# Kernel tuning notes

Hardware: AMD Instinct MI355X
Metric: run time of the kernel (lower is better)

Reference implementation:

```python
import jax, jax.numpy as jnp
import numpy as np

B, D, R = 16384, 4096, 64       # batch tokens, embed_dim, low_rank_dimension
N_PART = 8                       # number of subspace partitions
P = R // N_PART                  # partition size = 8
N_SEL = 4                        # partitions selected per example


def setup_inputs() -> dict:
    key = jax.random.key(0)
    k1, k2, k3, k4 = jax.random.split(key, 4)
    base = jax.random.normal(k1, (B, D), dtype=jnp.float32)
    source = jax.random.normal(k2, (B, D), dtype=jnp.float32)
    # orthogonal low-rank rotation (torch.nn.utils.parametrizations.orthogonal)
    W, _ = jnp.linalg.qr(jax.random.normal(k3, (D, R), dtype=jnp.float32))  # [D, R], orthonormal cols
    subspaces = jax.random.randint(k4, (B, N_SEL), 0, N_PART)               # partition ids per example
    return {"base": base, "source": source, "W": W, "subspaces": subspaces}


def reference(base, source, W, subspaces):
    # rotate into low-rank space: [B, R]
    rotated_base = base @ W
    rotated_source = source @ W
    diff = rotated_source - rotated_base

    # per-example selected rotated-space indices (contiguous partitions of size P)
    # idx[b] = concat over selected partitions of [p*P, p*P+P)
    idx = (subspaces[:, :, None] * P + jnp.arange(P)).reshape(B, N_SEL * P)  # [B, N_SEL*P]

    # Selecting columns of diff and matching rows of W.T, then matmul, is
    # equivalent to masking unselected rotated dims to zero and doing one GEMM.
    mask = jnp.zeros((B, R), dtype=diff.dtype).at[jnp.arange(B)[:, None], idx].set(1.0)
    output = base + (diff * mask) @ W.T  # [B, D]
    return output.astype(base.dtype)
```

## Files before the change

### kernel.cpp

```cpp
#include <hip/hip_runtime.h>


#define D_DIM 4096
#define R_DIM 64
#define BM1   16
#define BM2   32

typedef short bf16vec8 __attribute__((ext_vector_type(8)));
typedef float f32x4v  __attribute__((ext_vector_type(4)));

__device__ __forceinline__ unsigned int f2bf_u(float f) {
  unsigned int u = __builtin_bit_cast(unsigned int, f);
  return (u + 0x7fffu + ((u >> 16) & 1u)) >> 16;
}
__device__ __forceinline__ unsigned int pack2bf(float a, float b) {
  return f2bf_u(a) | (f2bf_u(b) << 16);
}
__device__ __forceinline__ void async_ld16(const void* g, void* l) {
  __builtin_amdgcn_global_load_lds(
      (const __attribute__((address_space(1))) void*)g,
      (__attribute__((address_space(3))) void*)l, 16, 0, 0);
}

__global__ __launch_bounds__(256)
void lrri_prep(const float* __restrict__ W, unsigned short* __restrict__ Wt,
               unsigned short* __restrict__ Wb) {
  const int idx = blockIdx.x * blockDim.x + threadIdx.x;
  const int k = idx >> 4;
  const int j = (idx & 15) * 4;
  float4 w = *(const float4*)(W + (size_t)k * R_DIM + j);
  ushort4 p;
  p.x = (unsigned short)f2bf_u(w.x);
  p.y = (unsigned short)f2bf_u(w.y);
  p.z = (unsigned short)f2bf_u(w.z);
  p.w = (unsigned short)f2bf_u(w.w);
  *(ushort4*)(Wb + (size_t)k * R_DIM + j) = p;
  Wt[(size_t)(j + 0) * D_DIM + k] = p.x;
  Wt[(size_t)(j + 1) * D_DIM + k] = p.y;
  Wt[(size_t)(j + 2) * D_DIM + k] = p.z;
  Wt[(size_t)(j + 3) * D_DIM + k] = p.w;
}

__global__ __launch_bounds__(512, 8)
void k1_rotdiff(const float* __restrict__ base, const float* __restrict__ srcp,
                const int* __restrict__ subs,
                const unsigned short* __restrict__ Wt_bf,
                unsigned short* __restrict__ rm_g)
{
  __shared__ __align__(16) float part[8][64 * 17];
  const int tid  = threadIdx.x;
  const int wave = tid >> 6;
  const int lane = tid & 63;
  const int l4   = lane & 15;
  const int g    = lane >> 4;
  const long rowbase = (long)blockIdx.x * BM1;
  const long rowA    = (rowbase + l4) * (long)D_DIM;
  const int  kq0     = wave * 512;
  const int  off1    = (blockIdx.x * 5) & 7;

  f32x4v acc[4];
  #pragma unroll
  for (int t = 0; t < 4; ++t) acc[t] = (f32x4v){0.f, 0.f, 0.f, 0.f};

  auto loadd = [&](int c, float4 (&vb)[4], float4 (&vs)[4]) {
    const int ch = (c + off1) & 7;
    const long colf = kq0 + ch * 64;
    #pragma unroll
    for (int q = 0; q < 4; ++q) {
      const long off = rowA + colf + (q >> 1) * 32 + g * 8 + (q & 1) * 4;
      vb[q] = *(const float4*)(base + off);
      vs[q] = *(const float4*)(srcp + off);
    }
  };

  auto comp = [&](int c, const float4 (&vb)[4], const float4 (&vs)[4]) {
    const int ch = (c + off1) & 7;
    const long colf = kq0 + ch * 64;
    uint4 df[2];
    #pragma unroll
    for (int s = 0; s < 2; ++s) {
      float d0 = vs[s*2].x - vb[s*2].x, d1 = vs[s*2].y - vb[s*2].y;
      float d2 = vs[s*2].z - vb[s*2].z, d3 = vs[s*2].w - vb[s*2].w;
      float d4 = vs[s*2+1].x - vb[s*2+1].x, d5 = vs[s*2+1].y - vb[s*2+1].y;
      float d6 = vs[s*2+1].z - vb[s*2+1].z, d7 = vs[s*2+1].w - vb[s*2+1].w;
      df[s].x = pack2bf(d0, d1);
      df[s].y = pack2bf(d2, d3);
      df[s].z = pack2bf(d4, d5);
      df[s].w = pack2bf(d6, d7);
    }
    #pragma unroll
    for (int t = 0; t < 4; ++t) {
      #pragma unroll
      for (int s = 0; s < 2; ++s) {
        uint4 wf = *(const uint4*)(Wt_bf + (size_t)(t * 16 + l4) * D_DIM +
                                   colf + s * 32 + g * 8);
        acc[t] = __builtin_amdgcn_mfma_f32_16x16x32_bf16(
            __builtin_bit_cast(bf16vec8, wf),
            __builtin_bit_cast(bf16vec8, df[s]),
            acc[t], 0, 0, 0);
      }
    }
  };

  float4 b0[4], s0[4], b1[4], s1[4];
  loadd(0, b0, s0);
  loadd(1, b1, s1); comp(0, b0, s0);
  loadd(2, b0, s0); comp(1, b1, s1);
  loadd(3, b1, s1); comp(2, b0, s0);
  loadd(4, b0, s0); comp(3, b1, s1);
  loadd(5, b1, s1); comp(4, b0, s0);
  loadd(6, b0, s0); comp(5, b1, s1);
  loadd(7, b1, s1); comp(6, b0, s0);
  comp(7, b1, s1);

  #pragma unroll
  for (int t = 0; t < 4; ++t)
    #pragma unroll
    for (int i = 0; i < 4; ++i)
      part[wave][(t * 16 + g * 4 + i) * 17 + l4] = acc[t][i];
  __syncthreads();

  {
    const int row = tid >> 5, jg = tid & 31;
    const int j0 = jg * 2;
    int4 sb = *(const int4*)(subs + (rowbase + row) * 4);
    unsigned mbits = (1u << sb.x) | (1u << sb.y) | (1u << sb.z) | (1u << sb.w);
    unsigned short v[2];
    #pragma unroll
    for (int jj = 0; jj < 2; ++jj) {
      const int j = j0 + jj;
      float sum = 0.f;
      #pragma unroll
      for (int w = 0; w < 8; ++w) sum += part[w][j * 17 + row];
      v[jj] = ((mbits >> (j >> 3)) & 1u) ? (unsigned short)f2bf_u(sum)
                                         : (unsigned short)0;
    }
    *(unsigned int*)(rm_g + (rowbase + row) * 64 + j0) =
        (unsigned)v[0] | ((unsigned)v[1] << 16);
  }
}

__global__ __launch_bounds__(256, 4)
void k2_apply(const float* __restrict__ base,
              const unsigned short* __restrict__ rm_g,
              const unsigned short* __restrict__ Wb_bf,
              float* __restrict__ out)
{
  __shared__ __align__(16) unsigned char smem[36864];
  const int tid  = threadIdx.x;
  const int wave = tid >> 6;
  const int lane = tid & 63;
  const int l4   = lane & 15;
  const int g    = lane >> 4;
  const long rowbase = (long)blockIdx.x * BM2;
  const int off2 = (blockIdx.x * 5) & 15;

  uint4 a2[2][2];
  #pragma unroll
  for (int m = 0; m < 2; ++m)
    #pragma unroll
    for (int s = 0; s < 2; ++s)
      a2[m][s] = *(const uint4*)(rm_g + (rowbase + m * 16 + l4) * 64 +
                                 s * 32 + g * 8);

  float* cbuf = (float*)(smem + wave * 9216);
  #pragma unroll 1
  for (int grp = 0; grp < 16; ++grp) {
    const int ga = (grp + off2) & 15;
    const int cbase = wave * 1024 + ga * 64;
    float4 bb[8];
    #pragma unroll
    for (int v2 = 0; v2 < 8; ++v2) {
      const int r = g + v2 * 4;
      bb[v2] = *(const float4*)(base + (rowbase + r) * D_DIM + cbase + l4 * 4);
    }
    f32x4v a[2][4];
    #pragma unroll
    for (int m = 0; m < 2; ++m)
      #pragma unroll
      for (int t = 0; t < 4; ++t) a[m][t] = (f32x4v){0.f, 0.f, 0.f, 0.f};
    #pragma unroll
    for (int t = 0; t < 4; ++t) {
      #pragma unroll
      for (int s = 0; s < 2; ++s) {
        uint4 bfrag = *(const uint4*)(Wb_bf +
            (size_t)(cbase + t * 16 + l4) * R_DIM + s * 32 + g * 8);
        #pragma unroll
        for (int m = 0; m < 2; ++m)
          a[m][t] = __builtin_amdgcn_mfma_f32_16x16x32_bf16(
              __builtin_bit_cast(bf16vec8, a2[m][s]),
              __builtin_bit_cast(bf16vec8, bfrag), a[m][t], 0, 0, 0);
      }
    }
    #pragma unroll
    for (int m = 0; m < 2; ++m)
      #pragma unroll
      for (int t = 0; t < 4; ++t)
        #pragma unroll
        for (int i = 0; i < 4; ++i)
          cbuf[(m * 16 + g * 4 + i) * 72 + t * 16 + l4] = a[m][t][i];
    __syncthreads();
    #pragma unroll
    for (int v2 = 0; v2 < 8; ++v2) {
      const int r = g + v2 * 4;
      f32x4v cv = *(const f32x4v*)(cbuf + r * 72 + l4 * 4);
      float4 o;
      o.x = cv[0] + bb[v2].x;
      o.y = cv[1] + bb[v2].y;
      o.z = cv[2] + bb[v2].z;
      o.w = cv[3] + bb[v2].w;
      *(float4*)(out + (rowbase + r) * D_DIM + cbase + l4 * 4) = o;
    }
    __syncthreads();
  }
}

__global__ __launch_bounds__(256, 2)
void lrri_fused_nows(const float* __restrict__ base, const float* __restrict__ srcp,
                     const float* __restrict__ W, const int* __restrict__ subs,
                     float* __restrict__ out)
{
  __shared__ __align__(16) unsigned char smem[70144];
  const int tid  = threadIdx.x;
  const int wave = tid >> 6;
  const int lane = tid & 63;
  const int l4   = lane & 15;
  const int g    = lane >> 4;
  const int rh   = wave >> 1;
  const int kh   = wave & 1;
  const long rowbase = (long)blockIdx.x * BM2;
  const long rowg    = rowbase + rh * 16;
  unsigned char* wbuf = smem + wave * 16384;
  const int off1 = (blockIdx.x * 7) & 63;
  const int off2 = (blockIdx.x * 5) & 15;

  f32x4v acc[4];
  #pragma unroll
  for (int t = 0; t < 4; ++t) acc[t] = (f32x4v){0.f, 0.f, 0.f, 0.f};

  #pragma unroll 1
  for (int c = 0; c < 64; ++c) {
    const int ch = (c + off1) & 63;
    unsigned char* buf = wbuf + (c & 1) * 8192;
    const long colf = kh * 2048 + ch * 32;
    #pragma unroll
    for (int q = 0; q < 2; ++q) {
      const int r = q * 8 + (lane >> 3);
      const unsigned b = ((unsigned)((lane & 7) * 16)) ^ ((unsigned)(r & 7) << 4);
      const long goff = (rowg + r) * (long)D_DIM + colf + (b >> 2);
      async_ld16(base + goff, buf + q * 1024);
      async_ld16(srcp + goff, buf + 2048 + q * 1024);
    }
    asm volatile("s_waitcnt vmcnt(0)" ::: "memory");
    __builtin_amdgcn_sched_barrier(0);
    const unsigned sw = (unsigned)((l4 & 7) << 4);
    const unsigned c0 = ((unsigned)(g * 32)) ^ sw;
    const unsigned c1 = ((unsigned)(g * 32 + 16)) ^ sw;
    float4 fb0 = *(const float4*)(buf + l4 * 128 + c0);
    float4 fb1 = *(const float4*)(buf + l4 * 128 + c1);
    float4 fs0 = *(const float4*)(buf + 2048 + l4 * 128 + c0);
    float4 fs1 = *(const float4*)(buf + 2048 + l4 * 128 + c1);
    uint4 af;
    af.x = pack2bf(fs0.x - fb0.x, fs0.y - fb0.y);
    af.y = pack2bf(fs0.z - fb0.z, fs0.w - fb0.w);
    af.z = pack2bf(fs1.x - fb1.x, fs1.y - fb1.y);
    af.w = pack2bf(fs1.z - fb1.z, fs1.w - fb1.w);
    #pragma unroll
    for (int t = 0; t < 4; ++t) {
      unsigned int pq[4];
      #pragma unroll
      for (int e2 = 0; e2 < 4; ++e2) {
        float wa = W[(size_t)(colf + g * 8 + e2 * 2    ) * R_DIM + t * 16 + l4];
        float wb = W[(size_t)(colf + g * 8 + e2 * 2 + 1) * R_DIM + t * 16 + l4];
        pq[e2] = pack2bf(wa, wb);
      }
      uint4 wf; wf.x = pq[0]; wf.y = pq[1]; wf.z = pq[2]; wf.w = pq[3];
      acc[t] = __builtin_amdgcn_mfma_f32_16x16x32_bf16(
          __builtin_bit_cast(bf16vec8, af),
          __builtin_bit_cast(bf16vec8, wf), acc[t], 0, 0, 0);
    }
  }

  {
    float* part = (float*)wbuf;
    #pragma unroll
    for (int t = 0; t < 4; ++t)
      #pragma unroll
      for (int i = 0; i < 4; ++i)
        part[(g * 4 + i) * 72 + t * 16 + l4] = acc[t][i];
  }
  __syncthreads();

  {
    const int row = tid >> 3, jg = tid & 7;
    const int lr  = row & 15;
    const float* pa = (const float*)(smem + ((row >> 4) * 2 + 0) * 16384);
    const float* pb = (const float*)(smem + ((row >> 4) * 2 + 1) * 16384);
    int4 sb = *(const int4*)(subs + (rowbase + row) * 4);
    unsigned mbits = (1u << sb.x) | (1u << sb.y) | (1u << sb.z) | (1u << sb.w);
    unsigned short v[8];
    #pragma unroll
    for (int jj = 0; jj < 8; ++jj) {
      const int j = jg * 8 + jj;
      float sum = pa[lr * 72 + j] + pb[lr * 72 + j];
      v[jj] = ((mbits >> (j >> 3)) & 1u) ? (unsigned short)f2bf_u(sum)
                                         : (unsigned short)0;
    }
    uint4 pk;
    pk.x = (unsigned)v[0] | ((unsigned)v[1] << 16);
    pk.y = (unsigned)v[2] | ((unsigned)v[3] << 16);
    pk.z = (unsigned)v[4] | ((unsigned)v[5] << 16);
    pk.w = (unsigned)v[6] | ((unsigned)v[7] << 16);
    *(uint4*)(smem + 65536 + row * 144 + jg * 16) = pk;
  }
  __syncthreads();

  uint4 a2[2][2];
  #pragma unroll
  for (int m = 0; m < 2; ++m)
    #pragma unroll
    for (int s = 0; s < 2; ++s)
      a2[m][s] = *(const uint4*)(smem + 65536 + (m * 16 + l4) * 144 +
                                 s * 64 + g * 16);
  float* cbuf = (float*)wbuf;
  #pragma unroll 1
  for (int grp = 0; grp < 16; ++grp) {
    const int ga = (grp + off2) & 15;
    const int cbase = wave * 1024 + ga * 64;
    float4 bb[8];
    #pragma unroll
    for (int v2 = 0; v2 < 8; ++v2) {
      const int r = g + v2 * 4;
      bb[v2] = *(const float4*)(base + (rowbase + r) * D_DIM + cbase + l4 * 4);
    }
    f32x4v a[2][4];
    #pragma unroll
    for (int m = 0; m < 2; ++m)
      #pragma unroll
      for (int t = 0; t < 4; ++t) a[m][t] = (f32x4v){0.f, 0.f, 0.f, 0.f};
    #pragma unroll
    for (int t = 0; t < 4; ++t) {
      #pragma unroll
      for (int s = 0; s < 2; ++s) {
        const float* wp = W + (size_t)(cbase + t * 16 + l4) * R_DIM + s * 32 + g * 8;
        float4 wa = *(const float4*)(wp);
        float4 wb2 = *(const float4*)(wp + 4);
        uint4 bfrag;
        bfrag.x = pack2bf(wa.x, wa.y); bfrag.y = pack2bf(wa.z, wa.w);
        bfrag.z = pack2bf(wb2.x, wb2.y); bfrag.w = pack2bf(wb2.z, wb2.w);
        #pragma unroll
        for (int m = 0; m < 2; ++m)
          a[m][t] = __builtin_amdgcn_mfma_f32_16x16x32_bf16(
              __builtin_bit_cast(bf16vec8, a2[m][s]),
              __builtin_bit_cast(bf16vec8, bfrag), a[m][t], 0, 0, 0);
      }
    }
    #pragma unroll
    for (int m = 0; m < 2; ++m)
      #pragma unroll
      for (int t = 0; t < 4; ++t)
        #pragma unroll
        for (int i = 0; i < 4; ++i)
          cbuf[(m * 16 + g * 4 + i) * 72 + t * 16 + l4] = a[m][t][i];
    #pragma unroll
    for (int v2 = 0; v2 < 8; ++v2) {
      const int r = g + v2 * 4;
      f32x4v cv = *(const f32x4v*)(cbuf + r * 72 + l4 * 4);
      float4 o;
      o.x = cv[0] + bb[v2].x;
      o.y = cv[1] + bb[v2].y;
      o.z = cv[2] + bb[v2].z;
      o.w = cv[3] + bb[v2].w;
      *(float4*)(out + (rowbase + r) * D_DIM + cbase + l4 * 4) = o;
    }
  }
}

extern "C" void kernel_launch(void* const* d_in, const int* in_sizes, int n_in,
                              void* d_out, int out_size, void* d_ws, size_t ws_size,
                              hipStream_t stream) {
  const float* base = (const float*)d_in[0];
  const float* srcp = (const float*)d_in[1];
  const float* W    = (const float*)d_in[2];
  const int*   subs = (const int*)d_in[3];
  float* out = (float*)d_out;

  const size_t wconv = (size_t)2 * R_DIM * D_DIM * sizeof(unsigned short);
  const size_t rmsz  = (size_t)16384 * R_DIM * sizeof(unsigned short);
  if (d_ws && ws_size >= wconv + rmsz) {
    unsigned short* Wt = (unsigned short*)d_ws;
    unsigned short* Wb = Wt + (size_t)R_DIM * D_DIM;
    unsigned short* rm = Wb + (size_t)R_DIM * D_DIM;
    lrri_prep<<<256, 256, 0, stream>>>(W, Wt, Wb);
    k1_rotdiff<<<16384 / BM1, 512, 0, stream>>>(base, srcp, subs, Wt, rm);
    k2_apply<<<16384 / BM2, 256, 0, stream>>>(base, rm, Wb, out);
  } else {
    lrri_fused_nows<<<16384 / BM2, 256, 0, stream>>>(base, srcp, W, subs, out);
  }
}
```

Baseline: 256.0 us.

## Fuse rotate and apply kernels into software-pipelined persistent block over tiles

Merges the rotation/diff kernel and the apply kernel into one kernel, so each block handles four 16-row tiles. The masked low-rank result moves through double-buffered LDS instead of a global scratch buffer. While the block computes the rotation for tile i+1, it interleaves the apply and output writes for tile i, overlapping the two phases' memory traffic. This removes a kernel launch and the global round trip. The cost is heavier per-block LDS use (about 76 KB) and lower occupancy (launch bounds 512,2), and base rows are still read twice.

```diff
diff --git a/kernel.cpp b/kernel.cpp
--- a/kernel.cpp
+++ b/kernel.cpp
@@ -3,7 +3,7 @@
 
 #define D_DIM 4096
 #define R_DIM 64
-#define BM1   16
+#define TPB   4
 #define BM2   32
 
 typedef short bf16vec8 __attribute__((ext_vector_type(8)));
@@ -41,29 +41,30 @@
   Wt[(size_t)(j + 3) * D_DIM + k] = p.w;
 }
 
-__global__ __launch_bounds__(512, 8)
-void k1_rotdiff(const float* __restrict__ base, const float* __restrict__ srcp,
-                const int* __restrict__ subs,
-                const unsigned short* __restrict__ Wt_bf,
-                unsigned short* __restrict__ rm_g)
+__global__ __launch_bounds__(512, 2)
+void lrri_pipe(const float* __restrict__ base, const float* __restrict__ srcp,
+               const int* __restrict__ subs,
+               const unsigned short* __restrict__ Wt_bf,
+               const unsigned short* __restrict__ Wb_bf,
+               float* __restrict__ out)
 {
   __shared__ __align__(16) float part[8][64 * 17];
+  __shared__ __align__(16) unsigned short rmb[2][16 * 64];
+  __shared__ __align__(16) float cbufs[8][16 * 72];
+
   const int tid  = threadIdx.x;
   const int wave = tid >> 6;
   const int lane = tid & 63;
   const int l4   = lane & 15;
   const int g    = lane >> 4;
-  const long rowbase = (long)blockIdx.x * BM1;
-  const long rowA    = (rowbase + l4) * (long)D_DIM;
-  const int  kq0     = wave * 512;
-  const int  off1    = (blockIdx.x * 5) & 7;
+  const int t0   = blockIdx.x * TPB;
+  const int kq0  = wave * 512;
+  float* cbuf = cbufs[wave];
 
   f32x4v acc[4];
-  #pragma unroll
-  for (int t = 0; t < 4; ++t) acc[t] = (f32x4v){0.f, 0.f, 0.f, 0.f};
-
-  auto loadd = [&](int c, float4 (&vb)[4], float4 (&vs)[4]) {
-    const int ch = (c + off1) & 7;
+
+  auto loadd = [&](int tile, int ch, float4 (&vb)[4], float4 (&vs)[4]) {
+    const long rowA = ((long)tile * 16 + l4) * (long)D_DIM;
     const long colf = kq0 + ch * 64;
     #pragma unroll
     for (int q = 0; q < 4; ++q) {
@@ -72,21 +73,15 @@
       vs[q] = *(const float4*)(srcp + off);
     }
   };
-
-  auto comp = [&](int c, const float4 (&vb)[4], const float4 (&vs)[4]) {
-    const int ch = (c + off1) & 7;
+  auto comp = [&](int ch, const float4 (&vb)[4], const float4 (&vs)[4]) {
     const long colf = kq0 + ch * 64;
     uint4 df[2];
     #pragma unroll
     for (int s = 0; s < 2; ++s) {
-      float d0 = vs[s*2].x - vb[s*2].x, d1 = vs[s*2].y - vb[s*2].y;
-      float d2 = vs[s*2].z - vb[s*2].z, d3 = vs[s*2].w - vb[s*2].w;
-      float d4 = vs[s*2+1].x - vb[s*2+1].x, d5 = vs[s*2+1].y - vb[s*2+1].y;
-      float d6 = vs[s*2+1].z - vb[s*2+1].z, d7 = vs[s*2+1].w - vb[s*2+1].w;
-      df[s].x = pack2bf(d0, d1);
-      df[s].y = pack2bf(d2, d3);
-      df[s].z = pack2bf(d4, d5);
-      df[s].w = pack2bf(d6, d7);
+      df[s].x = pack2bf(vs[s*2].x - vb[s*2].x, vs[s*2].y - vb[s*2].y);
+      df[s].y = pack2bf(vs[s*2].z - vb[s*2].z, vs[s*2].w - vb[s*2].w);
+      df[s].z = pack2bf(vs[s*2+1].x - vb[s*2+1].x, vs[s*2+1].y - vb[s*2+1].y);
+      df[s].w = pack2bf(vs[s*2+1].z - vb[s*2+1].z, vs[s*2+1].w - vb[s*2+1].w);
     }
     #pragma unroll
     for (int t = 0; t < 4; ++t) {
@@ -101,29 +96,16 @@
       }
     }
   };
-
-  float4 b0[4], s0[4], b1[4], s1[4];
-  loadd(0, b0, s0);
-  loadd(1, b1, s1); comp(0, b0, s0);
-  loadd(2, b0, s0); comp(1, b1, s1);
-  loadd(3, b1, s1); comp(2, b0, s0);
-  loadd(4, b0, s0); comp(3, b1, s1);
-  loadd(5, b1, s1); comp(4, b0, s0);
-  loadd(6, b0, s0); comp(5, b1, s1);
-  loadd(7, b1, s1); comp(6, b0, s0);
-  comp(7, b1, s1);
-
-  #pragma unroll
-  for (int t = 0; t < 4; ++t)
-    #pragma unroll
-    for (int i = 0; i < 4; ++i)
-      part[wave][(t * 16 + g * 4 + i) * 17 + l4] = acc[t][i];
-  __syncthreads();
-
-  {
-    const int row = tid >> 5, jg = tid & 31;
-    const int j0 = jg * 2;
-    int4 sb = *(const int4*)(subs + (rowbase + row) * 4);
+  auto savepart = [&]() {
+    #pragma unroll
+    for (int t = 0; t < 4; ++t)
+      #pragma unroll
+      for (int i = 0; i < 4; ++i)
+        part[wave][(t * 16 + g * 4 + i) * 17 + l4] = acc[t][i];
+  };
+  auto reduce = [&](int tile, int rbuf) {
+    const int row = tid >> 5, j0 = (tid & 31) * 2;
+    int4 sb = *(const int4*)(subs + (size_t)(tile * 16 + row) * 4);
     unsigned mbits = (1u << sb.x) | (1u << sb.y) | (1u << sb.z) | (1u << sb.w);
     unsigned short v[2];
     #pragma unroll
@@ -135,73 +117,40 @@
       v[jj] = ((mbits >> (j >> 3)) & 1u) ? (unsigned short)f2bf_u(sum)
                                          : (unsigned short)0;
     }
-    *(unsigned int*)(rm_g + (rowbase + row) * 64 + j0) =
+    *(unsigned int*)(&rmb[rbuf][row * 64 + j0]) =
         (unsigned)v[0] | ((unsigned)v[1] << 16);
-  }
-}
-
-__global__ __launch_bounds__(256, 4)
-void k2_apply(const float* __restrict__ base,
-              const unsigned short* __restrict__ rm_g,
-              const unsigned short* __restrict__ Wb_bf,
-              float* __restrict__ out)
-{
-  __shared__ __align__(16) unsigned char smem[36864];
-  const int tid  = threadIdx.x;
-  const int wave = tid >> 6;
-  const int lane = tid & 63;
-  const int l4   = lane & 15;
-  const int g    = lane >> 4;
-  const long rowbase = (long)blockIdx.x * BM2;
-  const int off2 = (blockIdx.x * 5) & 15;
-
-  uint4 a2[2][2];
-  #pragma unroll
-  for (int m = 0; m < 2; ++m)
-    #pragma unroll
-    for (int s = 0; s < 2; ++s)
-      a2[m][s] = *(const uint4*)(rm_g + (rowbase + m * 16 + l4) * 64 +
-                                 s * 32 + g * 8);
-
-  float* cbuf = (float*)(smem + wave * 9216);
-  #pragma unroll 1
-  for (int grp = 0; grp < 16; ++grp) {
-    const int ga = (grp + off2) & 15;
-    const int cbase = wave * 1024 + ga * 64;
-    float4 bb[8];
-    #pragma unroll
-    for (int v2 = 0; v2 < 8; ++v2) {
+  };
+
+  auto p2group = [&](int tile, int ga, const uint4 (&a2)[2]) {
+    const int cbase = kq0 + ga * 64;
+    const long rb = (long)tile * 16;
+    float4 bb[4];
+    #pragma unroll
+    for (int v2 = 0; v2 < 4; ++v2) {
       const int r = g + v2 * 4;
-      bb[v2] = *(const float4*)(base + (rowbase + r) * D_DIM + cbase + l4 * 4);
-    }
-    f32x4v a[2][4];
-    #pragma unroll
-    for (int m = 0; m < 2; ++m)
-      #pragma unroll
-      for (int t = 0; t < 4; ++t) a[m][t] = (f32x4v){0.f, 0.f, 0.f, 0.f};
+      bb[v2] = *(const float4*)(base + (rb + r) * (long)D_DIM + cbase + l4 * 4);
+    }
+    f32x4v a[4];
+    #pragma unroll
+    for (int t = 0; t < 4; ++t) a[t] = (f32x4v){0.f, 0.f, 0.f, 0.f};
     #pragma unroll
     for (int t = 0; t < 4; ++t) {
       #pragma unroll
       for (int s = 0; s < 2; ++s) {
         uint4 bfrag = *(const uint4*)(Wb_bf +
             (size_t)(cbase + t * 16 + l4) * R_DIM + s * 32 + g * 8);
-        #pragma unroll
-        for (int m = 0; m < 2; ++m)
-          a[m][t] = __builtin_amdgcn_mfma_f32_16x16x32_bf16(
-              __builtin_bit_cast(bf16vec8, a2[m][s]),
-              __builtin_bit_cast(bf16vec8, bfrag), a[m][t], 0, 0, 0);
+        a[t] = __builtin_amdgcn_mfma_f32_16x16x32_bf16(
+            __builtin_bit_cast(bf16vec8, a2[s]),
+            __builtin_bit_cast(bf16vec8, bfrag), a[t], 0, 0, 0);
       }
     }
     #pragma unroll
-    for (int m = 0; m < 2; ++m)
-      #pragma unroll
-      for (int t = 0; t < 4; ++t)
-        #pragma unroll
-        for (int i = 0; i < 4; ++i)
-          cbuf[(m * 16 + g * 4 + i) * 72 + t * 16 + l4] = a[m][t][i];
-    __syncthreads();
-    #pragma unroll
-    for (int v2 = 0; v2 < 8; ++v2) {
+    for (int t = 0; t < 4; ++t)
+      #pragma unroll
+      for (int i = 0; i < 4; ++i)
+        cbuf[(g * 4 + i) * 72 + t * 16 + l4] = a[t][i];
+    #pragma unroll
+    for (int v2 = 0; v2 < 4; ++v2) {
       const int r = g + v2 * 4;
       f32x4v cv = *(const f32x4v*)(cbuf + r * 72 + l4 * 4);
       float4 o;
@@ -209,9 +158,61 @@
       o.y = cv[1] + bb[v2].y;
       o.z = cv[2] + bb[v2].z;
       o.w = cv[3] + bb[v2].w;
-      *(float4*)(out + (rowbase + r) * D_DIM + cbase + l4 * 4) = o;
-    }
+      *(float4*)(out + (rb + r) * (long)D_DIM + cbase + l4 * 4) = o;
+    }
+  };
+
+  float4 vb[2][4], vs[2][4];
+
+  {
+    const int o1 = (blockIdx.x * 5) & 7;
+    #pragma unroll
+    for (int t = 0; t < 4; ++t) acc[t] = (f32x4v){0.f, 0.f, 0.f, 0.f};
+    loadd(t0, (0 + o1) & 7, vb[0], vs[0]);
+    #pragma unroll
+    for (int j = 0; j < 8; ++j) {
+      if (j < 7) loadd(t0, (j + 1 + o1) & 7, vb[(j + 1) & 1], vs[(j + 1) & 1]);
+      comp((j + o1) & 7, vb[j & 1], vs[j & 1]);
+    }
+    savepart();
+  }
+  __syncthreads();
+  reduce(t0, 0);
+  __syncthreads();
+
+  #pragma unroll 1
+  for (int i = 0; i < TPB - 1; ++i) {
+    uint4 a2[2];
+    #pragma unroll
+    for (int s = 0; s < 2; ++s)
+      a2[s] = *(const uint4*)(&rmb[i & 1][l4 * 64 + s * 32 + g * 8]);
+    #pragma unroll
+    for (int t = 0; t < 4; ++t) acc[t] = (f32x4v){0.f, 0.f, 0.f, 0.f};
+    const int o1 = (blockIdx.x * 5 + (i + 1) * 3) & 7;
+    const int o2 = (blockIdx.x * 3 + i) & 7;
+    loadd(t0 + i + 1, (0 + o1) & 7, vb[0], vs[0]);
+    #pragma unroll
+    for (int j = 0; j < 8; ++j) {
+      if (j < 7)
+        loadd(t0 + i + 1, (j + 1 + o1) & 7, vb[(j + 1) & 1], vs[(j + 1) & 1]);
+      p2group(t0 + i, (j + o2) & 7, a2);
+      comp((j + o1) & 7, vb[j & 1], vs[j & 1]);
+    }
+    savepart();
     __syncthreads();
+    reduce(t0 + i + 1, (i + 1) & 1);
+    __syncthreads();
+  }
+
+  {
+    uint4 a2[2];
+    #pragma unroll
+    for (int s = 0; s < 2; ++s)
+      a2[s] = *(const uint4*)(&rmb[(TPB - 1) & 1][l4 * 64 + s * 32 + g * 8]);
+    const int o2 = (blockIdx.x * 3 + (TPB - 1)) & 7;
+    #pragma unroll
+    for (int j = 0; j < 8; ++j)
+      p2group(t0 + TPB - 1, (j + o2) & 7, a2);
   }
 }
 
@@ -386,14 +387,12 @@
   float* out = (float*)d_out;
 
   const size_t wconv = (size_t)2 * R_DIM * D_DIM * sizeof(unsigned short);
-  const size_t rmsz  = (size_t)16384 * R_DIM * sizeof(unsigned short);
-  if (d_ws && ws_size >= wconv + rmsz) {
+  if (d_ws && ws_size >= wconv) {
     unsigned short* Wt = (unsigned short*)d_ws;
     unsigned short* Wb = Wt + (size_t)R_DIM * D_DIM;
-    unsigned short* rm = Wb + (size_t)R_DIM * D_DIM;
     lrri_prep<<<256, 256, 0, stream>>>(W, Wt, Wb);
-    k1_rotdiff<<<16384 / BM1, 512, 0, stream>>>(base, srcp, subs, Wt, rm);
-    k2_apply<<<16384 / BM2, 256, 0, stream>>>(base, rm, Wb, out);
+    lrri_pipe<<<16384 / (16 * TPB), 512, 0, stream>>>(base, srcp, subs,
+                                                      Wt, Wb, out);
   } else {
     lrri_fused_nows<<<16384 / BM2, 256, 0, stream>>>(base, srcp, W, subs, out);
   }
```

Measured after the change: 283.2 us. 10.6% more time.
